# Kernel optimization log

Measured on AMD Instinct MI355X. Metric: run time of the kernel, lower is better.

The kernel has to match this reference:

```python
import jax, jax.numpy as jnp
import numpy as np


def setup_inputs() -> dict:
    key = jax.random.key(0)
    ks = jax.random.split(key, 10)
    T, D, E, K, H = 16384, 1024, 8, 2, 4096
    scale = 0.02
    return {
        "x_flat": jax.random.normal(ks[0], (T, D), jnp.float32),
        "noise": jax.random.normal(ks[1], (T, E), jnp.float32),
        "gate_w": jax.random.normal(ks[2], (E, D), jnp.float32) * scale,
        "noise_weight": jnp.zeros((E,), jnp.float32),
        "w1": jax.random.normal(ks[3], (E, H, D), jnp.float32) * scale,
        "b1": jnp.zeros((E, H), jnp.float32),
        "w2": jax.random.normal(ks[4], (E, H, D), jnp.float32) * scale,
        "b2": jnp.zeros((E, H), jnp.float32),
        "wp": jax.random.normal(ks[5], (E, D, H), jnp.float32) * scale,
        "bp": jnp.zeros((E, D), jnp.float32),
    }


K_TOP = 2
LOAD_BALANCE_SCALE = 0.01


def reference(x_flat, noise, gate_w, noise_weight, w1, b1, w2, b2, wp, bp):
    T, D = x_flat.shape
    E = gate_w.shape[0]
    # ---- gate ----
    logits = x_flat @ gate_w.T                        # [T, E]
    gate_weights = jax.nn.softmax(logits, axis=-1)    # [T, E]
    gw_mean = gate_weights.mean(axis=0)               # [E]
    uniform = jnp.ones_like(gw_mean) / E
    load_balance_loss = jnp.mean((gw_mean - uniform) ** 2) * LOAD_BALANCE_SCALE
    # noisy top-k (noise_weight initialized to zeros => noise is a no-op, kept for faithfulness)
    logits_noisy = logits + noise * noise_weight
    top_v, top_i = jax.lax.top_k(logits_noisy, K_TOP)  # [T, K]
    neg_inf = jnp.full_like(logits_noisy, -jnp.inf)
    sparse = neg_inf.at[jnp.arange(T)[:, None], top_i].set(top_v)
    top_k_gated_weights = jax.nn.softmax(sparse, axis=-1)  # [T, E], zero off top-k
    # ---- experts (SwiGLU), weighted combine ----
    # Non-top-k weights are exactly 0, so a dense masked sum over experts equals
    # the original gather/grouped-GEMM/scatter dispatch on a single device.
    y = jnp.zeros_like(x_flat)
    for e in range(E):
        h = x_flat @ w1[e].T + b1[e]                  # [T, H]
        g = jax.nn.silu(x_flat @ w2[e].T + b2[e])     # [T, H]
        out_e = (h * g) @ wp[e].T + bp[e]             # [T, D]
        y = y + top_k_gated_weights[:, e:e + 1] * out_e
    return y, load_balance_loss
```

## Files before the change

kernel.cpp:

```cpp
#include <hip/hip_runtime.h>
#include <hip/hip_bf16.h>

#define T_TOK 16384
#define DDIM  1024
#define NEXP  8
#define HDIM  4096
#define HQ    1024
#define NQ    4

#define BM 128
#define BN 64
#define BK 64

typedef __attribute__((ext_vector_type(8))) short bf16x8;
typedef __attribute__((ext_vector_type(4))) float f32x4;

__device__ __forceinline__ unsigned short f2bf(float f) {
  unsigned int x = __builtin_bit_cast(unsigned int, f);
  x += 0x7fffu + ((x >> 16) & 1u);
  return (unsigned short)(x >> 16);
}
__device__ __forceinline__ void gload16(void* lds, const void* g) {
  __builtin_amdgcn_global_load_lds(
      (const __attribute__((address_space(1))) unsigned int*)g,
      (__attribute__((address_space(3))) unsigned int*)lds, 16, 0, 0);
}
__device__ __forceinline__ f32x4 mfma16(bf16x8 a, bf16x8 b, f32x4 c) {
  return __builtin_amdgcn_mfma_f32_16x16x32_bf16(a, b, c, 0, 0, 0);
}

#define OFF_GWSUM  ((size_t)0)
#define OFF_OFF16  ((size_t)64)
#define OFF_NP     ((size_t)128)
#define OFF_BLK    ((size_t)1024)
#define OFF_GBASE  ((size_t)8192)
#define OFF_PEXPP  ((size_t)16384)
#define OFF_PM0P   ((size_t)17408)
#define OFF_PENDP  ((size_t)18432)
#define OFF_PEXPS  ((size_t)19456)
#define OFF_PM0S   ((size_t)20480)
#define OFF_PENDS  ((size_t)21504)
#define OFF_TOPE   ((size_t)32768)
#define OFF_TOPW   (OFF_TOPE   + (size_t)T_TOK*2*4)
#define OFF_LRANK  (OFF_TOPW   + (size_t)T_TOK*2*4)
#define OFF_ROWTOK (OFF_LRANK  + (size_t)T_TOK*4)
#define OFF_ROWG   (OFF_ROWTOK + (size_t)T_TOK*2*4)
#define OFF_XG     ((size_t)1 << 20)
#define OFF_ACTQ   (OFF_XG   + (size_t)2*T_TOK*DDIM*2)
#define OFF_W1Q    (OFF_ACTQ + (size_t)2*T_TOK*HQ*2)
#define OFF_W2Q    (OFF_W1Q  + (size_t)NEXP*HQ*DDIM*2)
#define OFF_WPQ    (OFF_W2Q  + (size_t)NEXP*HQ*DDIM*2)
#define WS_NEEDED  (OFF_WPQ  + (size_t)NEXP*DDIM*HQ*2 + ((size_t)1<<20))

__global__ __launch_bounds__(256) void k_gate(
    const float* __restrict__ x, const float* __restrict__ noise,
    const float* __restrict__ gate_w, const float* __restrict__ nw,
    float* __restrict__ gwsum, int* __restrict__ tope, float* __restrict__ topw)
{
  __shared__ float gw_s[NEXP * DDIM];
  __shared__ float blk_gw[NEXP];
  const int tid = threadIdx.x;
  if (tid < NEXP) blk_gw[tid] = 0.f;
  {
    float4* dst = (float4*)gw_s;
    const float4* src = (const float4*)gate_w;
    for (int i = tid; i < NEXP * DDIM / 4; i += 256) dst[i] = src[i];
  }
  __syncthreads();

  const int wv = tid >> 6, lane = tid & 63;
  const int t = blockIdx.x * 4 + wv;

  const float4* xr = (const float4*)(x + (size_t)t * DDIM);
  float4 xv[4];
  #pragma unroll
  for (int c = 0; c < 4; ++c) xv[c] = xr[lane + 64 * c];

  float logit[NEXP];
  #pragma unroll
  for (int e = 0; e < NEXP; ++e) {
    float p = 0.f;
    const float4* g4 = (const float4*)(gw_s + e * DDIM);
    #pragma unroll
    for (int c = 0; c < 4; ++c) {
      float4 g = g4[lane + 64 * c];
      p += xv[c].x * g.x + xv[c].y * g.y + xv[c].z * g.z + xv[c].w * g.w;
    }
    #pragma unroll
    for (int off = 32; off >= 1; off >>= 1) p += __shfl_xor(p, off, 64);
    logit[e] = p;
  }

  if (lane == 0) {
    float m = logit[0];
    #pragma unroll
    for (int e = 1; e < NEXP; ++e) m = fmaxf(m, logit[e]);
    float sm[NEXP]; float s = 0.f;
    #pragma unroll
    for (int e = 0; e < NEXP; ++e) { sm[e] = expf(logit[e] - m); s += sm[e]; }
    float inv = 1.f / s;
    #pragma unroll
    for (int e = 0; e < NEXP; ++e) atomicAdd(&blk_gw[e], sm[e] * inv);

    float ln[NEXP];
    #pragma unroll
    for (int e = 0; e < NEXP; ++e) ln[e] = logit[e] + noise[(size_t)t * NEXP + e] * nw[e];
    int i1 = 0; float v1 = ln[0];
    #pragma unroll
    for (int e = 1; e < NEXP; ++e) if (ln[e] > v1) { v1 = ln[e]; i1 = e; }
    int i2 = -1; float v2 = -3.4e38f;
    #pragma unroll
    for (int e = 0; e < NEXP; ++e) if (e != i1 && ln[e] > v2) { v2 = ln[e]; i2 = e; }
    float b = expf(v2 - v1);
    float wsum = 1.f + b;
    tope[2 * t] = i1; tope[2 * t + 1] = i2;
    topw[2 * t] = 1.f / wsum; topw[2 * t + 1] = b / wsum;
  }
  __syncthreads();
  if (tid < NEXP) atomicAdd(&gwsum[tid], blk_gw[tid]);
}

__global__ __launch_bounds__(256) void k_hist(
    const int* __restrict__ tope, unsigned int* __restrict__ lrank,
    int* __restrict__ blkcnt)
{
  __shared__ int cnt16[16];
  const int tid = threadIdx.x;
  const int t = blockIdx.x * 256 + tid;
  if (tid < 16) cnt16[tid] = 0;
  __syncthreads();
  const int e0 = tope[2 * t], e1 = tope[2 * t + 1];
  const int b0 = 2 * e0 + (e0 < e1 ? 0 : 1);
  const int b1 = 2 * e1 + (e1 < e0 ? 0 : 1);
  const int lr0 = atomicAdd(&cnt16[b0], 1);
  const int lr1 = atomicAdd(&cnt16[b1], 1);
  lrank[t] = (unsigned int)lr0 | ((unsigned int)lr1 << 16);
  __syncthreads();
  if (tid < 16) blkcnt[blockIdx.x * 16 + tid] = cnt16[tid];
}

__global__ __launch_bounds__(512) void k_scan(
    const int* __restrict__ blkcnt, int* __restrict__ gbase,
    int* __restrict__ off16, int* __restrict__ np,
    int* __restrict__ pexpP, int* __restrict__ pm0P, int* __restrict__ pendP,
    int* __restrict__ pexpS, int* __restrict__ pm0S, int* __restrict__ pendS,
    const float* __restrict__ gwsum, float* __restrict__ out_loss)
{
  __shared__ int ld[64][16];
  __shared__ int sc[64][16];
  __shared__ int tot[16];
  __shared__ int o16[16];
  const int tid = threadIdx.x;
  for (int i = tid; i < 1024; i += 512) ld[i >> 4][i & 15] = blkcnt[i];
  __syncthreads();
  if (tid < 16) {
    int run = 0;
    for (int i = 0; i < 64; ++i) { sc[i][tid] = run; run += ld[i][tid]; }
    tot[tid] = run;
  }
  __syncthreads();
  if (tid == 0) {
    int o = 0;
    for (int b = 0; b < 16; ++b) { o16[b] = o; off16[b] = o; o += tot[b]; }
    int nP = 0, nS = 0;
    for (int b = 0; b < 16; ++b) {
      const int e = b >> 1, s = b & 1;
      const int beg = o16[b], end = beg + tot[b];
      for (int m = beg; m < end; m += BM) {
        const int me = (m + BM < end) ? (m + BM) : end;
        if (!s) { pexpP[nP] = e; pm0P[nP] = m; pendP[nP] = me; ++nP; }
        else    { pexpS[nS] = e; pm0S[nS] = m; pendS[nS] = me; ++nS; }
      }
    }
    np[0] = nP; np[1] = nS;
    float s = 0.f;
    for (int i = 0; i < NEXP; ++i) {
      float d = gwsum[i] / (float)T_TOK - 1.f / (float)NEXP;
      s += d * d;
    }
    out_loss[0] = (s / (float)NEXP) * 0.01f;
  }
  __syncthreads();
  for (int i = tid; i < 1024; i += 512)
    gbase[i] = o16[i & 15] + sc[i >> 4][i & 15];
}

__global__ __launch_bounds__(256) void k_copy(
    const float* __restrict__ x, const int* __restrict__ tope,
    const float* __restrict__ topw, const unsigned int* __restrict__ lrank,
    const int* __restrict__ gbase,
    int* __restrict__ rowtok, float* __restrict__ rowgate,
    unsigned short* __restrict__ Xg)
{
  const int tid = threadIdx.x;
  const int wv = tid >> 6, lane = tid & 63;
  const int t = blockIdx.x * 4 + wv;
  const int e0 = tope[2 * t], e1 = tope[2 * t + 1];
  const int b0 = 2 * e0 + (e0 < e1 ? 0 : 1);
  const int b1 = 2 * e1 + (e1 < e0 ? 0 : 1);
  const unsigned int lr = lrank[t];
  const int hb = t >> 8;
  const int r0 = gbase[hb * 16 + b0] + (int)(lr & 0xffffu);
  const int r1 = gbase[hb * 16 + b1] + (int)(lr >> 16);
  if (lane == 0) {
    rowtok[r0] = t; rowtok[r1] = t;
    rowgate[r0] = topw[2 * t]; rowgate[r1] = topw[2 * t + 1];
  }
  const float4* xr = (const float4*)(x + (size_t)t * DDIM);
  ushort4 o[4];
  #pragma unroll
  for (int c = 0; c < 4; ++c) {
    float4 v = xr[lane + 64 * c];
    o[c].x = f2bf(v.x); o[c].y = f2bf(v.y); o[c].z = f2bf(v.z); o[c].w = f2bf(v.w);
  }
  ushort4* d0 = (ushort4*)(Xg + (size_t)r0 * DDIM);
  ushort4* d1 = (ushort4*)(Xg + (size_t)r1 * DDIM);
  #pragma unroll
  for (int c = 0; c < 4; ++c) d0[lane + 64 * c] = o[c];
  #pragma unroll
  for (int c = 0; c < 4; ++c) d1[lane + 64 * c] = o[c];
}

__global__ __launch_bounds__(256) void k_castup(
    const float* __restrict__ w1, const float* __restrict__ w2,
    unsigned short* __restrict__ w1q, unsigned short* __restrict__ w2q, int q)
{
  const int N4 = NEXP * HQ * DDIM / 4;
  for (int i = blockIdx.x * 256 + threadIdx.x; i < 2 * N4; i += gridDim.x * 256) {
    const float* s; unsigned short* d; int j = i;
    if (j < N4) { s = w1; d = w1q; } else { s = w2; d = w2q; j -= N4; }
    const int c4 = j & 255;
    const int rr = j >> 8;
    const int e = rr >> 10, r = rr & 1023;
    float4 v = ((const float4*)s)[((size_t)e * HDIM + q * HQ + r) * 256 + c4];
    ushort4 o;
    o.x = f2bf(v.x); o.y = f2bf(v.y); o.z = f2bf(v.z); o.w = f2bf(v.w);
    ((ushort4*)d)[(size_t)rr * 256 + c4] = o;
  }
}

__global__ __launch_bounds__(256) void k_castdn(
    const float* __restrict__ wp, unsigned short* __restrict__ wpq, int q)
{
  const int N4 = NEXP * DDIM * HQ / 4;
  for (int i = blockIdx.x * 256 + threadIdx.x; i < N4; i += gridDim.x * 256) {
    const int c4 = i & 255;
    const int rr = i >> 8;
    float4 v = ((const float4*)wp)[(size_t)rr * 1024 + q * 256 + c4];
    ushort4 o;
    o.x = f2bf(v.x); o.y = f2bf(v.y); o.z = f2bf(v.z); o.w = f2bf(v.w);
    ((ushort4*)wpq)[(size_t)rr * 256 + c4] = o;
  }
}

#define FGX 280
#define FGY 16
__global__ __launch_bounds__(256, 2) void k_fused(
    const unsigned short* __restrict__ Xg,
    const unsigned short* __restrict__ w1q, const unsigned short* __restrict__ w2q,
    const float* __restrict__ b1, const float* __restrict__ b2,
    unsigned short* __restrict__ actq, const int* __restrict__ np,
    const int* __restrict__ pexpP, const int* __restrict__ pm0P, const int* __restrict__ pendP,
    const int* __restrict__ pexpS, const int* __restrict__ pm0S, const int* __restrict__ pendS,
    int q)
{
  const int flat = blockIdx.y * FGX + blockIdx.x;
  const int CPX = (FGX * FGY) / 8;
  const int L = (flat & 7) * CPX + (flat >> 3);
  const int pidx = L >> 4;
  const int yc = L & 15;
  const int nP = np[0], nS = np[1];
  int e, m0, mend;
  if (pidx < nP)            { e = pexpP[pidx]; m0 = pm0P[pidx]; mend = pendP[pidx]; }
  else if (pidx < nP + nS)  { int s = pidx - nP; e = pexpS[s]; m0 = pm0S[s]; mend = pendS[s]; }
  else return;

  __shared__ unsigned short As[BM * BK];
  __shared__ unsigned short B1s[BN * BK];
  __shared__ unsigned short B2s[BN * BK];

  const int tid = threadIdx.x;
  const int wid = tid >> 6, lane = tid & 63;
  const int wr = wid >> 1, wc = wid & 1;
  const int fr = lane & 15;
  const int fq = lane >> 4;

  const unsigned short* Bbase1 = w1q + ((size_t)e * HQ + yc * BN) * DDIM;
  const unsigned short* Bbase2 = w2q + ((size_t)e * HQ + yc * BN) * DDIM;

  f32x4 acc1[4][2] = {};
  f32x4 acc2[4][2] = {};

  for (int kt = 0; kt < DDIM / BK; ++kt) {
    if (kt > 0) __syncthreads();
    const int k0 = kt * BK;
    #pragma unroll
    for (int it = 0; it < 4; ++it) {
      const int idx = it * 256 + tid;
      const int row = idx >> 3, seg = idx & 7;
      const int koff = ((seg ^ (row & 7)) << 3);
      gload16(&As[idx * 8], Xg + (size_t)(m0 + row) * DDIM + k0 + koff);
    }
    #pragma unroll
    for (int it = 0; it < 2; ++it) {
      const int idx = it * 256 + tid;
      const int row = idx >> 3, seg = idx & 7;
      const int koff = ((seg ^ (row & 7)) << 3);
      gload16(&B1s[idx * 8], Bbase1 + (size_t)row * DDIM + k0 + koff);
    }
    #pragma unroll
    for (int it = 0; it < 2; ++it) {
      const int idx = it * 256 + tid;
      const int row = idx >> 3, seg = idx & 7;
      const int koff = ((seg ^ (row & 7)) << 3);
      gload16(&B2s[idx * 8], Bbase2 + (size_t)row * DDIM + k0 + koff);
    }
    __syncthreads();

    #pragma unroll
    for (int kk = 0; kk < 2; ++kk) {
      bf16x8 av[4], b1v[2], b2v[2];
      #pragma unroll
      for (int mf = 0; mf < 4; ++mf) {
        const int row = wr * 64 + mf * 16 + fr;
        const int seg = (kk * 4 + fq) ^ (row & 7);
        av[mf] = *(const bf16x8*)&As[row * BK + seg * 8];
      }
      #pragma unroll
      for (int nf = 0; nf < 2; ++nf) {
        const int row = wc * 32 + nf * 16 + fr;
        const int seg = (kk * 4 + fq) ^ (row & 7);
        b1v[nf] = *(const bf16x8*)&B1s[row * BK + seg * 8];
        b2v[nf] = *(const bf16x8*)&B2s[row * BK + seg * 8];
      }
      #pragma unroll
      for (int mf = 0; mf < 4; ++mf)
        #pragma unroll
        for (int nf = 0; nf < 2; ++nf) {
          acc1[mf][nf] = mfma16(av[mf], b1v[nf], acc1[mf][nf]);
          acc2[mf][nf] = mfma16(av[mf], b2v[nf], acc2[mf][nf]);
        }
    }
  }

  const int mcnt = mend - m0;
  #pragma unroll
  for (int mf = 0; mf < 4; ++mf) {
    const int rb = wr * 64 + mf * 16 + (fq << 2);
    #pragma unroll
    for (int nf = 0; nf < 2; ++nf) {
      const int cq = yc * BN + wc * 32 + nf * 16 + fr;
      const float bb1 = b1[(size_t)e * HDIM + q * HQ + cq];
      const float bb2 = b2[(size_t)e * HDIM + q * HQ + cq];
      #pragma unroll
      for (int j = 0; j < 4; ++j) {
        const int lr = rb + j;
        if (lr < mcnt) {
          float h = acc1[mf][nf][j] + bb1;
          float g = acc2[mf][nf][j] + bb2;
          float s = g / (1.f + expf(-g));
          actq[(size_t)(m0 + lr) * HQ + cq] = f2bf(h * s);
        }
      }
    }
  }
}

#define DGX 144
#define DGY 16
template<bool STORE>
__global__ __launch_bounds__(256, 2) void k_down(
    const unsigned short* __restrict__ actq, const unsigned short* __restrict__ wpq,
    const float* __restrict__ bp,
    const int* __restrict__ np, int npIdx,
    const int* __restrict__ pexp, const int* __restrict__ pm0, const int* __restrict__ pend,
    const int* __restrict__ rowtok, const float* __restrict__ rowgate,
    float* __restrict__ Y)
{
  const int flat = blockIdx.y * DGX + blockIdx.x;
  const int CPX = (DGX * DGY) / 8;
  const int L = (flat & 7) * CPX + (flat >> 3);
  const int pidx = L >> 4;
  const int yc = L & 15;
  if (pidx >= np[npIdx]) return;
  const int e = pexp[pidx], m0 = pm0[pidx], mend = pend[pidx];

  __shared__ unsigned short As[BM * BK];
  __shared__ unsigned short Bs[BN * BK];

  const int tid = threadIdx.x;
  const int wid = tid >> 6, lane = tid & 63;
  const int wr = wid >> 1, wc = wid & 1;
  const int fr = lane & 15;
  const int fq = lane >> 4;

  const unsigned short* Bbase = wpq + ((size_t)e * DDIM + yc * BN) * HQ;

  f32x4 acc[4][2] = {};

  for (int kt = 0; kt < HQ / BK; ++kt) {
    if (kt > 0) __syncthreads();
    const int k0 = kt * BK;
    #pragma unroll
    for (int it = 0; it < 4; ++it) {
      const int idx = it * 256 + tid;
      const int row = idx >> 3, seg = idx & 7;
      const int koff = ((seg ^ (row & 7)) << 3);
      gload16(&As[idx * 8], actq + (size_t)(m0 + row) * HQ + k0 + koff);
    }
    #pragma unroll
    for (int it = 0; it < 2; ++it) {
      const int idx = it * 256 + tid;
      const int row = idx >> 3, seg = idx & 7;
      const int koff = ((seg ^ (row & 7)) << 3);
      gload16(&Bs[idx * 8], Bbase + (size_t)row * HQ + k0 + koff);
    }
    __syncthreads();

    #pragma unroll
    for (int kk = 0; kk < 2; ++kk) {
      bf16x8 av[4], bv[2];
      #pragma unroll
      for (int mf = 0; mf < 4; ++mf) {
        const int row = wr * 64 + mf * 16 + fr;
        const int seg = (kk * 4 + fq) ^ (row & 7);
        av[mf] = *(const bf16x8*)&As[row * BK + seg * 8];
      }
      #pragma unroll
      for (int nf = 0; nf < 2; ++nf) {
        const int row = wc * 32 + nf * 16 + fr;
        const int seg = (kk * 4 + fq) ^ (row & 7);
        bv[nf] = *(const bf16x8*)&Bs[row * BK + seg * 8];
      }
      #pragma unroll
      for (int mf = 0; mf < 4; ++mf)
        #pragma unroll
        for (int nf = 0; nf < 2; ++nf)
          acc[mf][nf] = mfma16(av[mf], bv[nf], acc[mf][nf]);
    }
  }

  const int mcnt = mend - m0;
  #pragma unroll
  for (int mf = 0; mf < 4; ++mf) {
    const int rb = wr * 64 + mf * 16 + (fq << 2);
    #pragma unroll
    for (int nf = 0; nf < 2; ++nf) {
      const int dg = yc * BN + wc * 32 + nf * 16 + fr;
      const float bb = bp[(size_t)e * DDIM + dg];
      #pragma unroll
      for (int j = 0; j < 4; ++j) {
        const int lr = rb + j;
        if (lr < mcnt) {
          const int r = m0 + lr;
          const float o = rowgate[r] * (acc[mf][nf][j] + bb);
          float* yp = &Y[(size_t)rowtok[r] * DDIM + dg];
          if (STORE) *yp = o; else *yp += o;
        }
      }
    }
  }
}

extern "C" void kernel_launch(void* const* d_in, const int* in_sizes, int n_in,
                              void* d_out, int out_size, void* d_ws, size_t ws_size,
                              hipStream_t stream) {
  const float* x      = (const float*)d_in[0];
  const float* noise  = (const float*)d_in[1];
  const float* gate_w = (const float*)d_in[2];
  const float* nw     = (const float*)d_in[3];
  const float* w1     = (const float*)d_in[4];
  const float* b1     = (const float*)d_in[5];
  const float* w2     = (const float*)d_in[6];
  const float* b2     = (const float*)d_in[7];
  const float* wp     = (const float*)d_in[8];
  const float* bp     = (const float*)d_in[9];
  float* y = (float*)d_out;

  if (ws_size < WS_NEEDED) return;

  char* ws = (char*)d_ws;
  float* gwsum   = (float*)(ws + OFF_GWSUM);
  int*   off16   = (int*)(ws + OFF_OFF16);
  int*   np      = (int*)(ws + OFF_NP);
  int*   blkcnt  = (int*)(ws + OFF_BLK);
  int*   gbase   = (int*)(ws + OFF_GBASE);
  int*   pexpP   = (int*)(ws + OFF_PEXPP);
  int*   pm0P    = (int*)(ws + OFF_PM0P);
  int*   pendP   = (int*)(ws + OFF_PENDP);
  int*   pexpS   = (int*)(ws + OFF_PEXPS);
  int*   pm0S    = (int*)(ws + OFF_PM0S);
  int*   pendS   = (int*)(ws + OFF_PENDS);
  int*   tope    = (int*)(ws + OFF_TOPE);
  float* topw    = (float*)(ws + OFF_TOPW);
  unsigned int* lrank = (unsigned int*)(ws + OFF_LRANK);
  int*   rowtok  = (int*)(ws + OFF_ROWTOK);
  float* rowgate = (float*)(ws + OFF_ROWG);
  unsigned short* Xg   = (unsigned short*)(ws + OFF_XG);
  unsigned short* actq = (unsigned short*)(ws + OFF_ACTQ);
  unsigned short* w1q  = (unsigned short*)(ws + OFF_W1Q);
  unsigned short* w2q  = (unsigned short*)(ws + OFF_W2Q);
  unsigned short* wpq  = (unsigned short*)(ws + OFF_WPQ);

  hipMemsetAsync(d_ws, 0, 64, stream);

  k_gate<<<T_TOK / 4, 256, 0, stream>>>(x, noise, gate_w, nw, gwsum, tope, topw);
  k_hist<<<T_TOK / 256, 256, 0, stream>>>(tope, lrank, blkcnt);
  k_scan<<<1, 512, 0, stream>>>(blkcnt, gbase, off16, np,
                                pexpP, pm0P, pendP, pexpS, pm0S, pendS,
                                gwsum, y + (size_t)T_TOK * DDIM);
  k_copy<<<T_TOK / 4, 256, 0, stream>>>(x, tope, topw, lrank, gbase,
                                        rowtok, rowgate, Xg);

  for (int q = 0; q < NQ; ++q) {
    k_castup<<<2048, 256, 0, stream>>>(w1, w2, w1q, w2q, q);
    k_castdn<<<1024, 256, 0, stream>>>(wp, wpq, q);
    k_fused<<<dim3(FGX, FGY), 256, 0, stream>>>(
        Xg, w1q, w2q, b1, b2, actq, np,
        pexpP, pm0P, pendP, pexpS, pm0S, pendS, q);
    if (q == 0)
      k_down<true><<<dim3(DGX, DGY), 256, 0, stream>>>(
          actq, wpq, bp, np, 0, pexpP, pm0P, pendP, rowtok, rowgate, y);
    else
      k_down<false><<<dim3(DGX, DGY), 256, 0, stream>>>(
          actq, wpq, bp, np, 0, pexpP, pm0P, pendP, rowtok, rowgate, y);
    k_down<false><<<dim3(DGX, DGY), 256, 0, stream>>>(
        actq, wpq, bp, np, 1, pexpS, pm0S, pendS, rowtok, rowgate, y);
  }
}
```

Measured before the change: 1.694 ms.

## Use 256-row tiles with 512-thread blocks and merge weight-cast kernels

Raises the M tile to 256 rows and the block size to 512 threads (8 waves) for both the fused SwiGLU GEMM and the down-projection GEMM. It also narrows the fused kernel's N tile to 32 columns and regrids both launches. Each loaded B tile is now reused across more rows, and A rows past the end are clamped to the last valid row. The separate up and down weight-cast kernels are merged into one launch per quarter. The main risk is register pressure under launch_bounds(512,4), which could cause spills or lower occupancy.

```diff
diff --git a/kernel.cpp b/kernel.cpp
--- a/kernel.cpp
+++ b/kernel.cpp
@@ -7,9 +7,9 @@
 #define HDIM  4096
 #define HQ    1024
 #define NQ    4
-
-#define BM 128
-#define BN 64
+#define TOTR  (2 * T_TOK)
+
+#define BM 256
 #define BK 64
 
 typedef __attribute__((ext_vector_type(8))) short bf16x8;
@@ -46,8 +46,8 @@
 #define OFF_ROWTOK (OFF_LRANK  + (size_t)T_TOK*4)
 #define OFF_ROWG   (OFF_ROWTOK + (size_t)T_TOK*2*4)
 #define OFF_XG     ((size_t)1 << 20)
-#define OFF_ACTQ   (OFF_XG   + (size_t)2*T_TOK*DDIM*2)
-#define OFF_W1Q    (OFF_ACTQ + (size_t)2*T_TOK*HQ*2)
+#define OFF_ACTQ   (OFF_XG   + (size_t)TOTR*DDIM*2)
+#define OFF_W1Q    (OFF_ACTQ + (size_t)TOTR*HQ*2)
 #define OFF_W2Q    (OFF_W1Q  + (size_t)NEXP*HQ*DDIM*2)
 #define OFF_WPQ    (OFF_W2Q  + (size_t)NEXP*HQ*DDIM*2)
 #define WS_NEEDED  (OFF_WPQ  + (size_t)NEXP*DDIM*HQ*2 + ((size_t)1<<20))
@@ -221,41 +221,41 @@
   for (int c = 0; c < 4; ++c) d1[lane + 64 * c] = o[c];
 }
 
-__global__ __launch_bounds__(256) void k_castup(
+__global__ __launch_bounds__(256) void k_castall(
     const float* __restrict__ w1, const float* __restrict__ w2,
-    unsigned short* __restrict__ w1q, unsigned short* __restrict__ w2q, int q)
+    const float* __restrict__ wp,
+    unsigned short* __restrict__ w1q, unsigned short* __restrict__ w2q,
+    unsigned short* __restrict__ wpq, int q)
 {
   const int N4 = NEXP * HQ * DDIM / 4;
-  for (int i = blockIdx.x * 256 + threadIdx.x; i < 2 * N4; i += gridDim.x * 256) {
-    const float* s; unsigned short* d; int j = i;
-    if (j < N4) { s = w1; d = w1q; } else { s = w2; d = w2q; j -= N4; }
-    const int c4 = j & 255;
-    const int rr = j >> 8;
-    const int e = rr >> 10, r = rr & 1023;
-    float4 v = ((const float4*)s)[((size_t)e * HDIM + q * HQ + r) * 256 + c4];
+  for (int i = blockIdx.x * 256 + threadIdx.x; i < 3 * N4; i += gridDim.x * 256) {
+    int j = i;
+    float4 v; size_t dstIdx; unsigned short* d;
+    if (j < N4) {
+      const int c4 = j & 255, rr = j >> 8, e = rr >> 10, r = rr & 1023;
+      v = ((const float4*)w1)[((size_t)e * HDIM + q * HQ + r) * 256 + c4];
+      d = w1q; dstIdx = (size_t)rr * 256 + c4;
+    } else if (j < 2 * N4) {
+      j -= N4;
+      const int c4 = j & 255, rr = j >> 8, e = rr >> 10, r = rr & 1023;
+      v = ((const float4*)w2)[((size_t)e * HDIM + q * HQ + r) * 256 + c4];
+      d = w2q; dstIdx = (size_t)rr * 256 + c4;
+    } else {
+      j -= 2 * N4;
+      const int c4 = j & 255, rr = j >> 8;
+      v = ((const float4*)wp)[(size_t)rr * 1024 + q * 256 + c4];
+      d = wpq; dstIdx = (size_t)rr * 256 + c4;
+    }
     ushort4 o;
     o.x = f2bf(v.x); o.y = f2bf(v.y); o.z = f2bf(v.z); o.w = f2bf(v.w);
-    ((ushort4*)d)[(size_t)rr * 256 + c4] = o;
-  }
-}
-
-__global__ __launch_bounds__(256) void k_castdn(
-    const float* __restrict__ wp, unsigned short* __restrict__ wpq, int q)
-{
-  const int N4 = NEXP * DDIM * HQ / 4;
-  for (int i = blockIdx.x * 256 + threadIdx.x; i < N4; i += gridDim.x * 256) {
-    const int c4 = i & 255;
-    const int rr = i >> 8;
-    float4 v = ((const float4*)wp)[(size_t)rr * 1024 + q * 256 + c4];
-    ushort4 o;
-    o.x = f2bf(v.x); o.y = f2bf(v.y); o.z = f2bf(v.z); o.w = f2bf(v.w);
-    ((ushort4*)wpq)[(size_t)rr * 256 + c4] = o;
-  }
-}
-
-#define FGX 280
+    ((ushort4*)d)[dstIdx] = o;
+  }
+}
+
+#define FBN 32
+#define FGX 288
 #define FGY 16
-__global__ __launch_bounds__(256, 2) void k_fused(
+__global__ __launch_bounds__(512, 4) void k_fused(
     const unsigned short* __restrict__ Xg,
     const unsigned short* __restrict__ w1q, const unsigned short* __restrict__ w2q,
     const float* __restrict__ b1, const float* __restrict__ b2,
@@ -267,8 +267,8 @@
   const int flat = blockIdx.y * FGX + blockIdx.x;
   const int CPX = (FGX * FGY) / 8;
   const int L = (flat & 7) * CPX + (flat >> 3);
-  const int pidx = L >> 4;
-  const int yc = L & 15;
+  const int pidx = L >> 5;
+  const int yc = L & 31;
   const int nP = np[0], nS = np[1];
   int e, m0, mend;
   if (pidx < nP)            { e = pexpP[pidx]; m0 = pm0P[pidx]; mend = pendP[pidx]; }
@@ -276,8 +276,8 @@
   else return;
 
   __shared__ unsigned short As[BM * BK];
-  __shared__ unsigned short B1s[BN * BK];
-  __shared__ unsigned short B2s[BN * BK];
+  __shared__ unsigned short B1s[FBN * BK];
+  __shared__ unsigned short B2s[FBN * BK];
 
   const int tid = threadIdx.x;
   const int wid = tid >> 6, lane = tid & 63;
@@ -285,91 +285,75 @@
   const int fr = lane & 15;
   const int fq = lane >> 4;
 
-  const unsigned short* Bbase1 = w1q + ((size_t)e * HQ + yc * BN) * DDIM;
-  const unsigned short* Bbase2 = w2q + ((size_t)e * HQ + yc * BN) * DDIM;
-
-  f32x4 acc1[4][2] = {};
-  f32x4 acc2[4][2] = {};
+  const unsigned short* Bbase1 = w1q + ((size_t)e * HQ + yc * FBN) * DDIM;
+  const unsigned short* Bbase2 = w2q + ((size_t)e * HQ + yc * FBN) * DDIM;
+
+  f32x4 acc1[4] = {};
+  f32x4 acc2[4] = {};
+
+  const int bidx = tid & 255;
+  const int brow = bidx >> 3, bseg = bidx & 7;
+  const int bkoff = ((bseg ^ (brow & 7)) << 3);
 
   for (int kt = 0; kt < DDIM / BK; ++kt) {
     if (kt > 0) __syncthreads();
     const int k0 = kt * BK;
     #pragma unroll
     for (int it = 0; it < 4; ++it) {
-      const int idx = it * 256 + tid;
+      const int idx = it * 512 + tid;
       const int row = idx >> 3, seg = idx & 7;
       const int koff = ((seg ^ (row & 7)) << 3);
-      gload16(&As[idx * 8], Xg + (size_t)(m0 + row) * DDIM + k0 + koff);
-    }
-    #pragma unroll
-    for (int it = 0; it < 2; ++it) {
-      const int idx = it * 256 + tid;
-      const int row = idx >> 3, seg = idx & 7;
-      const int koff = ((seg ^ (row & 7)) << 3);
-      gload16(&B1s[idx * 8], Bbase1 + (size_t)row * DDIM + k0 + koff);
-    }
-    #pragma unroll
-    for (int it = 0; it < 2; ++it) {
-      const int idx = it * 256 + tid;
-      const int row = idx >> 3, seg = idx & 7;
-      const int koff = ((seg ^ (row & 7)) << 3);
-      gload16(&B2s[idx * 8], Bbase2 + (size_t)row * DDIM + k0 + koff);
-    }
+      int arow = m0 + row; if (arow >= TOTR) arow = TOTR - 1;
+      gload16(&As[idx * 8], Xg + (size_t)arow * DDIM + k0 + koff);
+    }
+    if (tid < 256)
+      gload16(&B1s[bidx * 8], Bbase1 + (size_t)brow * DDIM + k0 + bkoff);
+    else
+      gload16(&B2s[bidx * 8], Bbase2 + (size_t)brow * DDIM + k0 + bkoff);
     __syncthreads();
 
     #pragma unroll
     for (int kk = 0; kk < 2; ++kk) {
-      bf16x8 av[4], b1v[2], b2v[2];
+      const int browb = wc * 16 + fr;
+      const int bsegr = (kk * 4 + fq) ^ (browb & 7);
+      bf16x8 b1v = *(const bf16x8*)&B1s[browb * BK + bsegr * 8];
+      bf16x8 b2v = *(const bf16x8*)&B2s[browb * BK + bsegr * 8];
       #pragma unroll
       for (int mf = 0; mf < 4; ++mf) {
         const int row = wr * 64 + mf * 16 + fr;
         const int seg = (kk * 4 + fq) ^ (row & 7);
-        av[mf] = *(const bf16x8*)&As[row * BK + seg * 8];
+        bf16x8 av = *(const bf16x8*)&As[row * BK + seg * 8];
+        acc1[mf] = mfma16(av, b1v, acc1[mf]);
+        acc2[mf] = mfma16(av, b2v, acc2[mf]);
       }
-      #pragma unroll
-      for (int nf = 0; nf < 2; ++nf) {
-        const int row = wc * 32 + nf * 16 + fr;
-        const int seg = (kk * 4 + fq) ^ (row & 7);
-        b1v[nf] = *(const bf16x8*)&B1s[row * BK + seg * 8];
-        b2v[nf] = *(const bf16x8*)&B2s[row * BK + seg * 8];
-      }
-      #pragma unroll
-      for (int mf = 0; mf < 4; ++mf)
-        #pragma unroll
-        for (int nf = 0; nf < 2; ++nf) {
-          acc1[mf][nf] = mfma16(av[mf], b1v[nf], acc1[mf][nf]);
-          acc2[mf][nf] = mfma16(av[mf], b2v[nf], acc2[mf][nf]);
-        }
     }
   }
 
   const int mcnt = mend - m0;
+  const int cq = yc * FBN + wc * 16 + fr;
+  const float bb1 = b1[(size_t)e * HDIM + q * HQ + cq];
+  const float bb2 = b2[(size_t)e * HDIM + q * HQ + cq];
   #pragma unroll
   for (int mf = 0; mf < 4; ++mf) {
     const int rb = wr * 64 + mf * 16 + (fq << 2);
     #pragma unroll
-    for (int nf = 0; nf < 2; ++nf) {
-      const int cq = yc * BN + wc * 32 + nf * 16 + fr;
-      const float bb1 = b1[(size_t)e * HDIM + q * HQ + cq];
-      const float bb2 = b2[(size_t)e * HDIM + q * HQ + cq];
-      #pragma unroll
-      for (int j = 0; j < 4; ++j) {
-        const int lr = rb + j;
-        if (lr < mcnt) {
-          float h = acc1[mf][nf][j] + bb1;
-          float g = acc2[mf][nf][j] + bb2;
-          float s = g / (1.f + expf(-g));
-          actq[(size_t)(m0 + lr) * HQ + cq] = f2bf(h * s);
-        }
+    for (int j = 0; j < 4; ++j) {
+      const int lr = rb + j;
+      if (lr < mcnt) {
+        float h = acc1[mf][j] + bb1;
+        float g = acc2[mf][j] + bb2;
+        float s = g / (1.f + expf(-g));
+        actq[(size_t)(m0 + lr) * HQ + cq] = f2bf(h * s);
       }
     }
   }
 }
 
-#define DGX 144
+#define DBN 64
+#define DGX 80
 #define DGY 16
 template<bool STORE>
-__global__ __launch_bounds__(256, 2) void k_down(
+__global__ __launch_bounds__(512, 4) void k_down(
     const unsigned short* __restrict__ actq, const unsigned short* __restrict__ wpq,
     const float* __restrict__ bp,
     const int* __restrict__ np, int npIdx,
@@ -386,7 +370,7 @@
   const int e = pexp[pidx], m0 = pm0[pidx], mend = pend[pidx];
 
   __shared__ unsigned short As[BM * BK];
-  __shared__ unsigned short Bs[BN * BK];
+  __shared__ unsigned short Bs[DBN * BK];
 
   const int tid = threadIdx.x;
   const int wid = tid >> 6, lane = tid & 63;
@@ -394,7 +378,7 @@
   const int fr = lane & 15;
   const int fq = lane >> 4;
 
-  const unsigned short* Bbase = wpq + ((size_t)e * DDIM + yc * BN) * HQ;
+  const unsigned short* Bbase = wpq + ((size_t)e * DDIM + yc * DBN) * HQ;
 
   f32x4 acc[4][2] = {};
 
@@ -403,29 +387,22 @@
     const int k0 = kt * BK;
     #pragma unroll
     for (int it = 0; it < 4; ++it) {
-      const int idx = it * 256 + tid;
+      const int idx = it * 512 + tid;
       const int row = idx >> 3, seg = idx & 7;
       const int koff = ((seg ^ (row & 7)) << 3);
-      gload16(&As[idx * 8], actq + (size_t)(m0 + row) * HQ + k0 + koff);
-    }
-    #pragma unroll
-    for (int it = 0; it < 2; ++it) {
-      const int idx = it * 256 + tid;
-      const int row = idx >> 3, seg = idx & 7;
+      int arow = m0 + row; if (arow >= TOTR) arow = TOTR - 1;
+      gload16(&As[idx * 8], actq + (size_t)arow * HQ + k0 + koff);
+    }
+    {
+      const int row = tid >> 3, seg = tid & 7;
       const int koff = ((seg ^ (row & 7)) << 3);
-      gload16(&Bs[idx * 8], Bbase + (size_t)row * HQ + k0 + koff);
+      gload16(&Bs[tid * 8], Bbase + (size_t)row * HQ + k0 + koff);
     }
     __syncthreads();
 
     #pragma unroll
     for (int kk = 0; kk < 2; ++kk) {
-      bf16x8 av[4], bv[2];
-      #pragma unroll
-      for (int mf = 0; mf < 4; ++mf) {
-        const int row = wr * 64 + mf * 16 + fr;
-        const int seg = (kk * 4 + fq) ^ (row & 7);
-        av[mf] = *(const bf16x8*)&As[row * BK + seg * 8];
-      }
+      bf16x8 bv[2];
       #pragma unroll
       for (int nf = 0; nf < 2; ++nf) {
         const int row = wc * 32 + nf * 16 + fr;
@@ -433,10 +410,14 @@
         bv[nf] = *(const bf16x8*)&Bs[row * BK + seg * 8];
       }
       #pragma unroll
-      for (int mf = 0; mf < 4; ++mf)
+      for (int mf = 0; mf < 4; ++mf) {
+        const int row = wr * 64 + mf * 16 + fr;
+        const int seg = (kk * 4 + fq) ^ (row & 7);
+        bf16x8 av = *(const bf16x8*)&As[row * BK + seg * 8];
         #pragma unroll
         for (int nf = 0; nf < 2; ++nf)
-          acc[mf][nf] = mfma16(av[mf], bv[nf], acc[mf][nf]);
+          acc[mf][nf] = mfma16(av, bv[nf], acc[mf][nf]);
+      }
     }
   }
 
@@ -446,7 +427,7 @@
     const int rb = wr * 64 + mf * 16 + (fq << 2);
     #pragma unroll
     for (int nf = 0; nf < 2; ++nf) {
-      const int dg = yc * BN + wc * 32 + nf * 16 + fr;
+      const int dg = yc * DBN + wc * 32 + nf * 16 + fr;
       const float bb = bp[(size_t)e * DDIM + dg];
       #pragma unroll
       for (int j = 0; j < 4; ++j) {
@@ -513,18 +494,17 @@
                                         rowtok, rowgate, Xg);
 
   for (int q = 0; q < NQ; ++q) {
-    k_castup<<<2048, 256, 0, stream>>>(w1, w2, w1q, w2q, q);
-    k_castdn<<<1024, 256, 0, stream>>>(wp, wpq, q);
-    k_fused<<<dim3(FGX, FGY), 256, 0, stream>>>(
+    k_castall<<<3072, 256, 0, stream>>>(w1, w2, wp, w1q, w2q, wpq, q);
+    k_fused<<<dim3(FGX, FGY), 512, 0, stream>>>(
         Xg, w1q, w2q, b1, b2, actq, np,
         pexpP, pm0P, pendP, pexpS, pm0S, pendS, q);
     if (q == 0)
-      k_down<true><<<dim3(DGX, DGY), 256, 0, stream>>>(
+      k_down<true><<<dim3(DGX, DGY), 512, 0, stream>>>(
           actq, wpq, bp, np, 0, pexpP, pm0P, pendP, rowtok, rowgate, y);
     else
-      k_down<false><<<dim3(DGX, DGY), 256, 0, stream>>>(
+      k_down<false><<<dim3(DGX, DGY), 512, 0, stream>>>(
           actq, wpq, bp, np, 0, pexpP, pm0P, pendP, rowtok, rowgate, y);
-    k_down<false><<<dim3(DGX, DGY), 256, 0, stream>>>(
+    k_down<false><<<dim3(DGX, DGY), 512, 0, stream>>>(
         actq, wpq, bp, np, 1, pexpS, pm0S, pendS, rowtok, rowgate, y);
   }
 }
```

New measurement: 2.092 ms. 23.5% more time.

## Fuse fp32-to-bf16 weight casts into GEMM tile loads, drop cast kernels

Applied to the files above, without the earlier changes.

Removes the separate per-quarter weight cast kernels and instead has the fused up/gate GEMM and the down GEMM read fp32 weights directly, converting them to bf16 with packed convert instructions before storing into LDS. This eliminates the cast kernels' extra write and re-read of bf16 weight copies and the associated launches. The trade-off is that each GEMM tile now loads twice as many bytes of weights through registers instead of using async global-to-LDS loads, and every M-tile re-converts the same weights. The change also clamps A-row indices to the buffer end, moves A-fragment LDS reads inside the MFMA loop, and enlarges the gap between the partition-table offsets.

```diff
diff --git a/kernel.cpp b/kernel.cpp
--- a/kernel.cpp
+++ b/kernel.cpp
@@ -7,9 +7,9 @@
 #define HDIM  4096
 #define HQ    1024
 #define NQ    4
+#define TOTR  (2 * T_TOK)
 
 #define BM 128
-#define BN 64
 #define BK 64
 
 typedef __attribute__((ext_vector_type(8))) short bf16x8;
@@ -27,6 +27,17 @@
 }
 __device__ __forceinline__ f32x4 mfma16(bf16x8 a, bf16x8 b, f32x4 c) {
   return __builtin_amdgcn_mfma_f32_16x16x32_bf16(a, b, c, 0, 0, 0);
+}
+__device__ __forceinline__ void pack8_store(unsigned short* dst, const float* s) {
+  float4 a = ((const float4*)s)[0];
+  float4 b = ((const float4*)s)[1];
+  unsigned int p0, p1, p2, p3;
+  asm("v_cvt_pk_bf16_f32 %0, %1, %2" : "=v"(p0) : "v"(a.x), "v"(a.y));
+  asm("v_cvt_pk_bf16_f32 %0, %1, %2" : "=v"(p1) : "v"(a.z), "v"(a.w));
+  asm("v_cvt_pk_bf16_f32 %0, %1, %2" : "=v"(p2) : "v"(b.x), "v"(b.y));
+  asm("v_cvt_pk_bf16_f32 %0, %1, %2" : "=v"(p3) : "v"(b.z), "v"(b.w));
+  uint4 pk; pk.x = p0; pk.y = p1; pk.z = p2; pk.w = p3;
+  *(uint4*)dst = pk;
 }
 
 #define OFF_GWSUM  ((size_t)0)
@@ -35,22 +46,19 @@
 #define OFF_BLK    ((size_t)1024)
 #define OFF_GBASE  ((size_t)8192)
 #define OFF_PEXPP  ((size_t)16384)
-#define OFF_PM0P   ((size_t)17408)
-#define OFF_PENDP  ((size_t)18432)
-#define OFF_PEXPS  ((size_t)19456)
-#define OFF_PM0S   ((size_t)20480)
-#define OFF_PENDS  ((size_t)21504)
+#define OFF_PM0P   ((size_t)18432)
+#define OFF_PENDP  ((size_t)20480)
+#define OFF_PEXPS  ((size_t)22528)
+#define OFF_PM0S   ((size_t)24576)
+#define OFF_PENDS  ((size_t)26624)
 #define OFF_TOPE   ((size_t)32768)
 #define OFF_TOPW   (OFF_TOPE   + (size_t)T_TOK*2*4)
 #define OFF_LRANK  (OFF_TOPW   + (size_t)T_TOK*2*4)
 #define OFF_ROWTOK (OFF_LRANK  + (size_t)T_TOK*4)
 #define OFF_ROWG   (OFF_ROWTOK + (size_t)T_TOK*2*4)
 #define OFF_XG     ((size_t)1 << 20)
-#define OFF_ACTQ   (OFF_XG   + (size_t)2*T_TOK*DDIM*2)
-#define OFF_W1Q    (OFF_ACTQ + (size_t)2*T_TOK*HQ*2)
-#define OFF_W2Q    (OFF_W1Q  + (size_t)NEXP*HQ*DDIM*2)
-#define OFF_WPQ    (OFF_W2Q  + (size_t)NEXP*HQ*DDIM*2)
-#define WS_NEEDED  (OFF_WPQ  + (size_t)NEXP*DDIM*HQ*2 + ((size_t)1<<20))
+#define OFF_ACTQ   (OFF_XG   + (size_t)TOTR*DDIM*2)
+#define WS_NEEDED  (OFF_ACTQ + (size_t)TOTR*HQ*2 + ((size_t)1<<20))
 
 __global__ __launch_bounds__(256) void k_gate(
     const float* __restrict__ x, const float* __restrict__ noise,
@@ -221,43 +229,12 @@
   for (int c = 0; c < 4; ++c) d1[lane + 64 * c] = o[c];
 }
 
-__global__ __launch_bounds__(256) void k_castup(
-    const float* __restrict__ w1, const float* __restrict__ w2,
-    unsigned short* __restrict__ w1q, unsigned short* __restrict__ w2q, int q)
-{
-  const int N4 = NEXP * HQ * DDIM / 4;
-  for (int i = blockIdx.x * 256 + threadIdx.x; i < 2 * N4; i += gridDim.x * 256) {
-    const float* s; unsigned short* d; int j = i;
-    if (j < N4) { s = w1; d = w1q; } else { s = w2; d = w2q; j -= N4; }
-    const int c4 = j & 255;
-    const int rr = j >> 8;
-    const int e = rr >> 10, r = rr & 1023;
-    float4 v = ((const float4*)s)[((size_t)e * HDIM + q * HQ + r) * 256 + c4];
-    ushort4 o;
-    o.x = f2bf(v.x); o.y = f2bf(v.y); o.z = f2bf(v.z); o.w = f2bf(v.w);
-    ((ushort4*)d)[(size_t)rr * 256 + c4] = o;
-  }
-}
-
-__global__ __launch_bounds__(256) void k_castdn(
-    const float* __restrict__ wp, unsigned short* __restrict__ wpq, int q)
-{
-  const int N4 = NEXP * DDIM * HQ / 4;
-  for (int i = blockIdx.x * 256 + threadIdx.x; i < N4; i += gridDim.x * 256) {
-    const int c4 = i & 255;
-    const int rr = i >> 8;
-    float4 v = ((const float4*)wp)[(size_t)rr * 1024 + q * 256 + c4];
-    ushort4 o;
-    o.x = f2bf(v.x); o.y = f2bf(v.y); o.z = f2bf(v.z); o.w = f2bf(v.w);
-    ((ushort4*)wpq)[(size_t)rr * 256 + c4] = o;
-  }
-}
-
+#define FBN 64
 #define FGX 280
 #define FGY 16
 __global__ __launch_bounds__(256, 2) void k_fused(
     const unsigned short* __restrict__ Xg,
-    const unsigned short* __restrict__ w1q, const unsigned short* __restrict__ w2q,
+    const float* __restrict__ w1, const float* __restrict__ w2,
     const float* __restrict__ b1, const float* __restrict__ b2,
     unsigned short* __restrict__ actq, const int* __restrict__ np,
     const int* __restrict__ pexpP, const int* __restrict__ pm0P, const int* __restrict__ pendP,
@@ -276,8 +253,8 @@
   else return;
 
   __shared__ unsigned short As[BM * BK];
-  __shared__ unsigned short B1s[BN * BK];
-  __shared__ unsigned short B2s[BN * BK];
+  __shared__ unsigned short B1s[FBN * BK];
+  __shared__ unsigned short B2s[FBN * BK];
 
   const int tid = threadIdx.x;
   const int wid = tid >> 6, lane = tid & 63;
@@ -285,11 +262,14 @@
   const int fr = lane & 15;
   const int fq = lane >> 4;
 
-  const unsigned short* Bbase1 = w1q + ((size_t)e * HQ + yc * BN) * DDIM;
-  const unsigned short* Bbase2 = w2q + ((size_t)e * HQ + yc * BN) * DDIM;
+  const float* W1f = w1 + ((size_t)e * HDIM + (size_t)q * HQ + yc * FBN) * DDIM;
+  const float* W2f = w2 + ((size_t)e * HDIM + (size_t)q * HQ + yc * FBN) * DDIM;
 
   f32x4 acc1[4][2] = {};
   f32x4 acc2[4][2] = {};
+
+  const int brow = tid >> 3, bseg = tid & 7;
+  const int bkoff = ((bseg ^ (brow & 7)) << 3);
 
   for (int kt = 0; kt < DDIM / BK; ++kt) {
     if (kt > 0) __syncthreads();
@@ -299,33 +279,28 @@
       const int idx = it * 256 + tid;
       const int row = idx >> 3, seg = idx & 7;
       const int koff = ((seg ^ (row & 7)) << 3);
-      gload16(&As[idx * 8], Xg + (size_t)(m0 + row) * DDIM + k0 + koff);
+      int arow = m0 + row; if (arow >= TOTR) arow = TOTR - 1;
+      gload16(&As[idx * 8], Xg + (size_t)arow * DDIM + k0 + koff);
     }
     #pragma unroll
     for (int it = 0; it < 2; ++it) {
       const int idx = it * 256 + tid;
-      const int row = idx >> 3, seg = idx & 7;
-      const int koff = ((seg ^ (row & 7)) << 3);
-      gload16(&B1s[idx * 8], Bbase1 + (size_t)row * DDIM + k0 + koff);
+      const int row = (it * 256 + tid) >> 3 ? (idx >> 3) : brow;
+      const int seg = idx & 7;
+      const int koff = ((seg ^ ((idx >> 3) & 7)) << 3);
+      pack8_store(&B1s[idx * 8], W1f + (size_t)(idx >> 3) * DDIM + k0 + koff);
     }
     #pragma unroll
     for (int it = 0; it < 2; ++it) {
       const int idx = it * 256 + tid;
-      const int row = idx >> 3, seg = idx & 7;
-      const int koff = ((seg ^ (row & 7)) << 3);
-      gload16(&B2s[idx * 8], Bbase2 + (size_t)row * DDIM + k0 + koff);
+      const int koff = (((idx & 7) ^ ((idx >> 3) & 7)) << 3);
+      pack8_store(&B2s[idx * 8], W2f + (size_t)(idx >> 3) * DDIM + k0 + koff);
     }
     __syncthreads();
 
     #pragma unroll
     for (int kk = 0; kk < 2; ++kk) {
-      bf16x8 av[4], b1v[2], b2v[2];
-      #pragma unroll
-      for (int mf = 0; mf < 4; ++mf) {
-        const int row = wr * 64 + mf * 16 + fr;
-        const int seg = (kk * 4 + fq) ^ (row & 7);
-        av[mf] = *(const bf16x8*)&As[row * BK + seg * 8];
-      }
+      bf16x8 b1v[2], b2v[2];
       #pragma unroll
       for (int nf = 0; nf < 2; ++nf) {
         const int row = wc * 32 + nf * 16 + fr;
@@ -334,12 +309,16 @@
         b2v[nf] = *(const bf16x8*)&B2s[row * BK + seg * 8];
       }
       #pragma unroll
-      for (int mf = 0; mf < 4; ++mf)
+      for (int mf = 0; mf < 4; ++mf) {
+        const int row = wr * 64 + mf * 16 + fr;
+        const int seg = (kk * 4 + fq) ^ (row & 7);
+        bf16x8 av = *(const bf16x8*)&As[row * BK + seg * 8];
         #pragma unroll
         for (int nf = 0; nf < 2; ++nf) {
-          acc1[mf][nf] = mfma16(av[mf], b1v[nf], acc1[mf][nf]);
-          acc2[mf][nf] = mfma16(av[mf], b2v[nf], acc2[mf][nf]);
+          acc1[mf][nf] = mfma16(av, b1v[nf], acc1[mf][nf]);
+          acc2[mf][nf] = mfma16(av, b2v[nf], acc2[mf][nf]);
         }
+      }
     }
   }
 
@@ -349,7 +328,7 @@
     const int rb = wr * 64 + mf * 16 + (fq << 2);
     #pragma unroll
     for (int nf = 0; nf < 2; ++nf) {
-      const int cq = yc * BN + wc * 32 + nf * 16 + fr;
+      const int cq = yc * FBN + wc * 32 + nf * 16 + fr;
       const float bb1 = b1[(size_t)e * HDIM + q * HQ + cq];
       const float bb2 = b2[(size_t)e * HDIM + q * HQ + cq];
       #pragma unroll
@@ -366,16 +345,17 @@
   }
 }
 
+#define DBN 64
 #define DGX 144
 #define DGY 16
 template<bool STORE>
 __global__ __launch_bounds__(256, 2) void k_down(
-    const unsigned short* __restrict__ actq, const unsigned short* __restrict__ wpq,
+    const unsigned short* __restrict__ actq, const float* __restrict__ wp,
     const float* __restrict__ bp,
     const int* __restrict__ np, int npIdx,
     const int* __restrict__ pexp, const int* __restrict__ pm0, const int* __restrict__ pend,
     const int* __restrict__ rowtok, const float* __restrict__ rowgate,
-    float* __restrict__ Y)
+    float* __restrict__ Y, int q)
 {
   const int flat = blockIdx.y * DGX + blockIdx.x;
   const int CPX = (DGX * DGY) / 8;
@@ -386,7 +366,7 @@
   const int e = pexp[pidx], m0 = pm0[pidx], mend = pend[pidx];
 
   __shared__ unsigned short As[BM * BK];
-  __shared__ unsigned short Bs[BN * BK];
+  __shared__ unsigned short Bs[DBN * BK];
 
   const int tid = threadIdx.x;
   const int wid = tid >> 6, lane = tid & 63;
@@ -394,7 +374,7 @@
   const int fr = lane & 15;
   const int fq = lane >> 4;
 
-  const unsigned short* Bbase = wpq + ((size_t)e * DDIM + yc * BN) * HQ;
+  const float* Wpf = wp + ((size_t)e * DDIM + yc * DBN) * HDIM + (size_t)q * HQ;
 
   f32x4 acc[4][2] = {};
 
@@ -406,26 +386,20 @@
       const int idx = it * 256 + tid;
       const int row = idx >> 3, seg = idx & 7;
       const int koff = ((seg ^ (row & 7)) << 3);
-      gload16(&As[idx * 8], actq + (size_t)(m0 + row) * HQ + k0 + koff);
+      int arow = m0 + row; if (arow >= TOTR) arow = TOTR - 1;
+      gload16(&As[idx * 8], actq + (size_t)arow * HQ + k0 + koff);
     }
     #pragma unroll
     for (int it = 0; it < 2; ++it) {
       const int idx = it * 256 + tid;
-      const int row = idx >> 3, seg = idx & 7;
-      const int koff = ((seg ^ (row & 7)) << 3);
-      gload16(&Bs[idx * 8], Bbase + (size_t)row * HQ + k0 + koff);
+      const int koff = (((idx & 7) ^ ((idx >> 3) & 7)) << 3);
+      pack8_store(&Bs[idx * 8], Wpf + (size_t)(idx >> 3) * HDIM + k0 + koff);
     }
     __syncthreads();
 
     #pragma unroll
     for (int kk = 0; kk < 2; ++kk) {
-      bf16x8 av[4], bv[2];
-      #pragma unroll
-      for (int mf = 0; mf < 4; ++mf) {
-        const int row = wr * 64 + mf * 16 + fr;
-        const int seg = (kk * 4 + fq) ^ (row & 7);
-        av[mf] = *(const bf16x8*)&As[row * BK + seg * 8];
-      }
+      bf16x8 bv[2];
       #pragma unroll
       for (int nf = 0; nf < 2; ++nf) {
         const int row = wc * 32 + nf * 16 + fr;
@@ -433,10 +407,14 @@
         bv[nf] = *(const bf16x8*)&Bs[row * BK + seg * 8];
       }
       #pragma unroll
-      for (int mf = 0; mf < 4; ++mf)
+      for (int mf = 0; mf < 4; ++mf) {
+        const int row = wr * 64 + mf * 16 + fr;
+        const int seg = (kk * 4 + fq) ^ (row & 7);
+        bf16x8 av = *(const bf16x8*)&As[row * BK + seg * 8];
         #pragma unroll
         for (int nf = 0; nf < 2; ++nf)
-          acc[mf][nf] = mfma16(av[mf], bv[nf], acc[mf][nf]);
+          acc[mf][nf] = mfma16(av, bv[nf], acc[mf][nf]);
+      }
     }
   }
 
@@ -446,7 +424,7 @@
     const int rb = wr * 64 + mf * 16 + (fq << 2);
     #pragma unroll
     for (int nf = 0; nf < 2; ++nf) {
-      const int dg = yc * BN + wc * 32 + nf * 16 + fr;
+      const int dg = yc * DBN + wc * 32 + nf * 16 + fr;
       const float bb = bp[(size_t)e * DDIM + dg];
       #pragma unroll
       for (int j = 0; j < 4; ++j) {
@@ -498,9 +476,6 @@
   float* rowgate = (float*)(ws + OFF_ROWG);
   unsigned short* Xg   = (unsigned short*)(ws + OFF_XG);
   unsigned short* actq = (unsigned short*)(ws + OFF_ACTQ);
-  unsigned short* w1q  = (unsigned short*)(ws + OFF_W1Q);
-  unsigned short* w2q  = (unsigned short*)(ws + OFF_W2Q);
-  unsigned short* wpq  = (unsigned short*)(ws + OFF_WPQ);
 
   hipMemsetAsync(d_ws, 0, 64, stream);
 
@@ -513,18 +488,16 @@
                                         rowtok, rowgate, Xg);
 
   for (int q = 0; q < NQ; ++q) {
-    k_castup<<<2048, 256, 0, stream>>>(w1, w2, w1q, w2q, q);
-    k_castdn<<<1024, 256, 0, stream>>>(wp, wpq, q);
     k_fused<<<dim3(FGX, FGY), 256, 0, stream>>>(
-        Xg, w1q, w2q, b1, b2, actq, np,
+        Xg, w1, w2, b1, b2, actq, np,
         pexpP, pm0P, pendP, pexpS, pm0S, pendS, q);
     if (q == 0)
       k_down<true><<<dim3(DGX, DGY), 256, 0, stream>>>(
-          actq, wpq, bp, np, 0, pexpP, pm0P, pendP, rowtok, rowgate, y);
+          actq, wp, bp, np, 0, pexpP, pm0P, pendP, rowtok, rowgate, y, q);
     else
       k_down<false><<<dim3(DGX, DGY), 256, 0, stream>>>(
-          actq, wpq, bp, np, 0, pexpP, pm0P, pendP, rowtok, rowgate, y);
+          actq, wp, bp, np, 0, pexpP, pm0P, pendP, rowtok, rowgate, y, q);
     k_down<false><<<dim3(DGX, DGY), 256, 0, stream>>>(
-        actq, wpq, bp, np, 1, pexpS, pm0S, pendS, rowtok, rowgate, y);
-  }
-}
+        actq, wp, bp, np, 1, pexpS, pm0S, pendS, rowtok, rowgate, y, q);
+  }
+}
```

Result: slower. 1.926 ms (+13.7%).
